# Kernel optimization log

Hardware: AMD Instinct MI355X
Metric: run time of the kernel (lower is better)

The kernel has to match this reference:

```python
import jax, jax.numpy as jnp
import numpy as np

N_NODES = 100000
N_EDGES = 1600000
IN_FEATS = 128
H_FEATS = 128


def setup_inputs() -> dict:
    key = jax.random.key(0)
    ks = jax.random.split(key, 8)
    s_in = 1.0 / np.sqrt(IN_FEATS)
    s_h = 1.0 / np.sqrt(H_FEATS)
    return {
        "emb_weight": jax.random.normal(ks[0], (N_NODES, IN_FEATS), jnp.float32),
        "W1_self": jax.random.normal(ks[1], (IN_FEATS, H_FEATS), jnp.float32) * s_in,
        "W1_neigh": jax.random.normal(ks[2], (IN_FEATS, H_FEATS), jnp.float32) * s_in,
        "b1": jnp.zeros((H_FEATS,), jnp.float32),
        "W2_self": jax.random.normal(ks[3], (H_FEATS, H_FEATS), jnp.float32) * s_h,
        "W2_neigh": jax.random.normal(ks[4], (H_FEATS, H_FEATS), jnp.float32) * s_h,
        "b2": jnp.zeros((H_FEATS,), jnp.float32),
        "edges": jax.random.randint(ks[5], (2, N_EDGES), 0, N_NODES, jnp.int64)
            if jax.config.jax_enable_x64 else
            jax.random.randint(ks[5], (2, N_EDGES), 0, N_NODES, jnp.int32),
    }


def _sage_conv(h, src, dst, W_self, W_neigh, b):
    # DGL SAGEConv(mean): out = h @ W_self + mean_neigh(h) @ W_neigh + b
    agg = jax.ops.segment_sum(h[src], dst, num_segments=N_NODES)  # [N, F]
    deg = jax.ops.segment_sum(jnp.ones((src.shape[0],), h.dtype), dst,
                              num_segments=N_NODES)
    mean = agg / jnp.maximum(deg, 1.0)[:, None]  # zero-in-degree -> zeros
    return h @ W_self + mean @ W_neigh + b


def reference(emb_weight, W1_self, W1_neigh, b1, W2_self, W2_neigh, b2, edges):
    src, dst = edges[0], edges[1]
    h = emb_weight  # node_emb(g.nodes()) over all nodes
    h = _sage_conv(h, src, dst, W1_self, W1_neigh, b1)
    h = jax.nn.leaky_relu(h, negative_slope=0.2)
    # dropout is identity in eval mode
    h = _sage_conv(h, src, dst, W2_self, W2_neigh, b2)
    return h
```

## Files before the change

### kernel.cpp

```cpp
#include <hip/hip_runtime.h>
#include <hip/hip_bf16.h>

#define N_NODES_C 100000
#define FEATS 128
#define SH 10
#define NBK 128
#define PB  256
#define CAST_BLOCKS 12500

typedef unsigned int uint32;
typedef __bf16 bf16_t;
typedef bf16_t bf16x8 __attribute__((ext_vector_type(8)));
typedef float f32x4 __attribute__((ext_vector_type(4)));

union Frag { uint4 u; bf16x8 v; };

__device__ __forceinline__ unsigned short f32_to_bf16_bits(float f) {
    uint32 u = __float_as_uint(f);
    u += 0x7fffu + ((u >> 16) & 1u);
    return (unsigned short)(u >> 16);
}
__device__ __forceinline__ float bf16_lo(uint32 p) { return __uint_as_float(p << 16); }
__device__ __forceinline__ float bf16_hi(uint32 p) { return __uint_as_float(p & 0xffff0000u); }

__global__ __launch_bounds__(256) void prep_fused(
    const int* __restrict__ dst, int* __restrict__ gHist, int nE, int chunk,
    const float4* __restrict__ emb4, unsigned short* __restrict__ hb0, int n4,
    const float* __restrict__ W1s, const float* __restrict__ W1n, unsigned short* __restrict__ wt1,
    const float* __restrict__ W2s, const float* __restrict__ W2n, unsigned short* __restrict__ wt2)
{
    __shared__ int h[NBK];
    const int b = blockIdx.x;
    const int tid = threadIdx.x;

    if (b < PB) {
        if (tid < NBK) h[tid] = 0;
        __syncthreads();
        const int b0 = b * chunk;
        const int e1 = min(b0 + chunk, nE);
        for (int e = b0 + tid; e < e1; e += 256)
            atomicAdd(&h[dst[e] >> SH], 1);
        __syncthreads();
        if (tid < NBK) gHist[tid * PB + b] = h[tid];
    } else if (b < PB + 32) {
        const int which = (b - PB) >> 4;
        const float* Ws = which ? W2s : W1s;
        const float* Wn = which ? W2n : W1n;
        unsigned short* wt = which ? wt2 : wt1;
        int gid = ((b - PB) & 15) * 256 + tid;
        int frag = gid >> 6, lane = gid & 63;
        int nt = frag >> 3, ks = frag & 7;
        int n = nt * 16 + (lane & 15);
        int kbase = ks * 32 + (lane >> 4) * 8;
        union { unsigned short s[8]; uint4 u; } o;
#pragma unroll
        for (int j = 0; j < 8; ++j) {
            int k = kbase + j;
            float v = (k < 128) ? Ws[(size_t)k * FEATS + n] : Wn[(size_t)(k - 128) * FEATS + n];
            o.s[j] = f32_to_bf16_bits(v);
        }
        *(uint4*)(wt + (size_t)gid * 8) = o.u;
    } else {
        int i = (b - PB - 32) * 256 + tid;
        if (i >= n4) return;
        float4 v = emb4[i];
        union { unsigned short s[4]; uint2 u; } o;
        o.s[0] = f32_to_bf16_bits(v.x);
        o.s[1] = f32_to_bf16_bits(v.y);
        o.s[2] = f32_to_bf16_bits(v.z);
        o.s[3] = f32_to_bf16_bits(v.w);
        *(uint2*)(hb0 + (size_t)i * 4) = o.u;
    }
}

__global__ __launch_bounds__(1024) void scan_one(int* __restrict__ g) {
    __shared__ int ss[1024];
    const int tid = threadIdx.x;
    const int base = tid * 32;
    int pref[32];
    int sum = 0;
#pragma unroll
    for (int j = 0; j < 32; ++j) {
        int v = g[base + j];
        pref[j] = sum;
        sum += v;
    }
    ss[tid] = sum;
    __syncthreads();
    for (int d = 1; d < 1024; d <<= 1) {
        int t = (tid >= d) ? ss[tid - d] : 0;
        __syncthreads();
        ss[tid] += t;
        __syncthreads();
    }
    int ex = ss[tid] - sum;
#pragma unroll
    for (int j = 0; j < 32; ++j)
        g[base + j] = ex + pref[j];
}

__global__ __launch_bounds__(256) void part_scatter(const int* __restrict__ src,
                                                    const int* __restrict__ dst,
                                                    const int* __restrict__ gScan,
                                                    uint32* __restrict__ ebuf,
                                                    int nE, int chunk) {
    __shared__ int cur[NBK];
    const int tid = threadIdx.x;
    if (tid < NBK) cur[tid] = gScan[tid * PB + blockIdx.x];
    __syncthreads();
    const int b0 = blockIdx.x * chunk;
    const int e1 = min(b0 + chunk, nE);
    for (int e = b0 + tid; e < e1; e += 256) {
        int d = dst[e];
        int pos = atomicAdd(&cur[d >> SH], 1);
        ebuf[pos] = (uint32)src[e] | ((uint32)(d & ((1 << SH) - 1)) << 17);
    }
}

__global__ __launch_bounds__(1024) void bucket_csr(const uint32* __restrict__ ebuf,
                                                   const int* __restrict__ gScan,
                                                   int* __restrict__ off,
                                                   int* __restrict__ csr,
                                                   int nE) {
    __shared__ int cnt[1 << SH];
    __shared__ int ss[1 << SH];
    const int b = blockIdx.x;
    const int tid = threadIdx.x;
    const int start = gScan[b * PB];
    const int end = gScan[(b + 1) * PB];
    const int nodeBase = b << SH;
    cnt[tid] = 0;
    __syncthreads();
    for (int e = start + tid; e < end; e += 1024)
        atomicAdd(&cnt[ebuf[e] >> 17], 1);
    __syncthreads();
    int own = cnt[tid];
    ss[tid] = own;
    __syncthreads();
    for (int d = 1; d < 1024; d <<= 1) {
        int t = (tid >= d) ? ss[tid - d] : 0;
        __syncthreads();
        ss[tid] += t;
        __syncthreads();
    }
    int ex = ss[tid] - own;
    cnt[tid] = ex;
    int node = nodeBase + tid;
    if (node < N_NODES_C) off[node] = start + ex;
    if (b == gridDim.x - 1 && tid == 0) off[N_NODES_C] = nE;
    __syncthreads();
    for (int e = start + tid; e < end; e += 1024) {
        uint32 p = ebuf[e];
        int pos = atomicAdd(&cnt[p >> 17], 1);
        csr[start + pos] = (int)((p & 0x1FFFFu) << 8);
    }
}

__global__ __launch_bounds__(256) void gather_mean_w2(const unsigned short* __restrict__ hb,
                                                      const int* __restrict__ csrB,
                                                      const int* __restrict__ off,
                                                      unsigned short* __restrict__ meanb,
                                                      int nNodes) {
    const int node = blockIdx.x * 4 + (threadIdx.x >> 6);
    const int lane = threadIdx.x & 63;
    if (node >= nNodes) return;
    const int start = __builtin_amdgcn_readfirstlane(off[node]);
    const int end   = __builtin_amdgcn_readfirstlane(off[node + 1]);
    const int half = lane >> 5;
    const int c = lane & 31;
    const char* base = (const char*)hb + (size_t)(c * 8);
    float a0 = 0.f, a1 = 0.f, a2 = 0.f, a3 = 0.f;
    int e = start;
    for (; e + 8 <= end; e += 8) {
        const int o0 = csrB[e + 0], o1 = csrB[e + 1], o2 = csrB[e + 2], o3 = csrB[e + 3];
        const int o4 = csrB[e + 4], o5 = csrB[e + 5], o6 = csrB[e + 6], o7 = csrB[e + 7];
        const uint2 u0 = *(const uint2*)(base + (size_t)(half ? o1 : o0));
        const uint2 u1 = *(const uint2*)(base + (size_t)(half ? o3 : o2));
        const uint2 u2 = *(const uint2*)(base + (size_t)(half ? o5 : o4));
        const uint2 u3 = *(const uint2*)(base + (size_t)(half ? o7 : o6));
        a0 += bf16_lo(u0.x); a1 += bf16_hi(u0.x); a2 += bf16_lo(u0.y); a3 += bf16_hi(u0.y);
        a0 += bf16_lo(u1.x); a1 += bf16_hi(u1.x); a2 += bf16_lo(u1.y); a3 += bf16_hi(u1.y);
        a0 += bf16_lo(u2.x); a1 += bf16_hi(u2.x); a2 += bf16_lo(u2.y); a3 += bf16_hi(u2.y);
        a0 += bf16_lo(u3.x); a1 += bf16_hi(u3.x); a2 += bf16_lo(u3.y); a3 += bf16_hi(u3.y);
    }
    if (e + 4 <= end) {
        const int o0 = csrB[e + 0], o1 = csrB[e + 1], o2 = csrB[e + 2], o3 = csrB[e + 3];
        const uint2 u0 = *(const uint2*)(base + (size_t)(half ? o1 : o0));
        const uint2 u1 = *(const uint2*)(base + (size_t)(half ? o3 : o2));
        a0 += bf16_lo(u0.x); a1 += bf16_hi(u0.x); a2 += bf16_lo(u0.y); a3 += bf16_hi(u0.y);
        a0 += bf16_lo(u1.x); a1 += bf16_hi(u1.x); a2 += bf16_lo(u1.y); a3 += bf16_hi(u1.y);
        e += 4;
    }
    if (e + 2 <= end) {
        const int o0 = csrB[e + 0], o1 = csrB[e + 1];
        const uint2 u = *(const uint2*)(base + (size_t)(half ? o1 : o0));
        a0 += bf16_lo(u.x); a1 += bf16_hi(u.x); a2 += bf16_lo(u.y); a3 += bf16_hi(u.y);
        e += 2;
    }
    if (e < end && half == 0) {
        const uint2 u = *(const uint2*)(base + (size_t)csrB[e]);
        a0 += bf16_lo(u.x); a1 += bf16_hi(u.x); a2 += bf16_lo(u.y); a3 += bf16_hi(u.y);
    }
    a0 += __shfl_xor(a0, 32);
    a1 += __shfl_xor(a1, 32);
    a2 += __shfl_xor(a2, 32);
    a3 += __shfl_xor(a3, 32);
    const int deg = end - start;
    const float invd = (deg > 0) ? (1.f / (float)deg) : 0.f;
    if (half == 0) {
        uint2 o;
        o.x = ((uint32)f32_to_bf16_bits(a1 * invd) << 16) | (uint32)f32_to_bf16_bits(a0 * invd);
        o.y = ((uint32)f32_to_bf16_bits(a3 * invd) << 16) | (uint32)f32_to_bf16_bits(a2 * invd);
        ((uint2*)meanb)[(size_t)node * 32 + c] = o;
    }
}

__global__ __launch_bounds__(256) void sage_gemm_mfma(const unsigned short* __restrict__ HB,
                                                      const unsigned short* __restrict__ MB,
                                                      const unsigned short* __restrict__ WT,
                                                      const float* __restrict__ bias,
                                                      void* __restrict__ OUTP,
                                                      int nNodes, int mode) {
    const int wave = threadIdx.x >> 6;
    const int lane = threadIdx.x & 63;
    const int waveBase = blockIdx.x * 64 + wave * 16;
    const int m = lane & 15;
    const int quad = lane >> 4;

    int arow = waveBase + m;
    if (arow >= nNodes) arow = nNodes - 1;
    const uint4* hrow = (const uint4*)(HB + (size_t)arow * FEATS);
    const uint4* mrow = (const uint4*)(MB + (size_t)arow * FEATS);

    Frag a[8];
#pragma unroll
    for (int ks = 0; ks < 4; ++ks) a[ks].u = hrow[ks * 4 + quad];
#pragma unroll
    for (int ks = 0; ks < 4; ++ks) a[ks + 4].u = mrow[ks * 4 + quad];

    const uint4* wt4 = (const uint4*)WT;
    f32x4 acc[8];
#pragma unroll
    for (int nt = 0; nt < 8; ++nt) acc[nt] = (f32x4){0.f, 0.f, 0.f, 0.f};

#pragma unroll
    for (int ks = 0; ks < 8; ++ks) {
#pragma unroll
        for (int nt = 0; nt < 8; ++nt) {
            Frag b;
            b.u = wt4[(size_t)(nt * 8 + ks) * 64 + lane];
            acc[nt] = __builtin_amdgcn_mfma_f32_16x16x32_bf16(a[ks].v, b.v, acc[nt], 0, 0, 0);
        }
    }

#pragma unroll
    for (int nt = 0; nt < 8; ++nt) {
        const int col = nt * 16 + m;
        const float bv = bias[col];
#pragma unroll
        for (int r = 0; r < 4; ++r) {
            const int grow = waveBase + quad * 4 + r;
            if (grow >= nNodes) continue;
            float v = acc[nt][r] + bv;
            if (mode) {
                v = v > 0.f ? v : 0.2f * v;
                ((unsigned short*)OUTP)[(size_t)grow * FEATS + col] = f32_to_bf16_bits(v);
            } else {
                ((float*)OUTP)[(size_t)grow * FEATS + col] = v;
            }
        }
    }
}

extern "C" void kernel_launch(void* const* d_in, const int* in_sizes, int n_in,
                              void* d_out, int out_size, void* d_ws, size_t ws_size,
                              hipStream_t stream) {
    const float* emb = (const float*)d_in[0];
    const float* W1s = (const float*)d_in[1];
    const float* W1n = (const float*)d_in[2];
    const float* b1  = (const float*)d_in[3];
    const float* W2s = (const float*)d_in[4];
    const float* W2n = (const float*)d_in[5];
    const float* b2  = (const float*)d_in[6];
    const int*   edg = (const int*)d_in[7];

    const int nE = in_sizes[7] / 2;
    const int* src = edg;
    const int* dst = edg + nE;

    const int chunk = (nE + PB - 1) / PB;
    const int nActB = (N_NODES_C + (1 << SH) - 1) >> SH;
    const int n4 = N_NODES_C * FEATS / 4;

    const size_t bfTab = (size_t)N_NODES_C * FEATS * sizeof(unsigned short);

    char* ws = (char*)d_ws;
    int* off      = (int*)(ws);
    int* gHist    = (int*)(ws + (512 << 10));
    int* csr      = (int*)(ws + (1 << 20));
    uint32* ebuf  = (uint32*)(ws + (8 << 20));
    unsigned short* wt1 = (unsigned short*)(ws + (15 << 20));
    unsigned short* wt2 = (unsigned short*)(ws + (15 << 20) + (64 << 10));
    unsigned short* hb0 = (unsigned short*)(ws + (16 << 20));
    unsigned short* h1b = (unsigned short*)((char*)hb0 + bfTab);
    unsigned short* mnb = (unsigned short*)((char*)h1b + bfTab);
    float* out = (float*)d_out;

    prep_fused<<<PB + 32 + CAST_BLOCKS, 256, 0, stream>>>(
        dst, gHist, nE, chunk, (const float4*)emb, hb0, n4,
        W1s, W1n, wt1, W2s, W2n, wt2);

    scan_one<<<1, 1024, 0, stream>>>(gHist);
    part_scatter<<<PB, 256, 0, stream>>>(src, dst, gHist, ebuf, nE, chunk);
    bucket_csr<<<nActB, 1024, 0, stream>>>(ebuf, gHist, off, csr, nE);

    const int gatherBlocks = (N_NODES_C + 3) / 4;
    const int gemmBlocks = (N_NODES_C + 63) / 64;

    gather_mean_w2<<<gatherBlocks, 256, 0, stream>>>(hb0, csr, off, mnb, N_NODES_C);
    sage_gemm_mfma<<<gemmBlocks, 256, 0, stream>>>(hb0, mnb, wt1, b1, h1b, N_NODES_C, 1);

    gather_mean_w2<<<gatherBlocks, 256, 0, stream>>>(h1b, csr, off, mnb, N_NODES_C);
    sage_gemm_mfma<<<gemmBlocks, 256, 0, stream>>>(h1b, mnb, wt2, b2, out, N_NODES_C, 0);
}
```

Before: 349.3 us.

## Widen scatter blocks, unroll gather by 16, and compute two row tiles per GEMM wave

Three independent changes. The partition scatter now runs 1024 threads per block instead of 256, giving more parallelism per chunk. The neighbor gather loop is unrolled to 16 edges per iteration so more independent loads are in flight. The MFMA GEMM now has each wave handle 32 rows (two 16-row tiles) that share each weight fragment load, halving the weight traffic per row at the cost of more registers and half as many blocks.

```diff
diff --git a/kernel.cpp b/kernel.cpp
--- a/kernel.cpp
+++ b/kernel.cpp
@@ -99,18 +99,18 @@
         g[base + j] = ex + pref[j];
 }
 
-__global__ __launch_bounds__(256) void part_scatter(const int* __restrict__ src,
-                                                    const int* __restrict__ dst,
-                                                    const int* __restrict__ gScan,
-                                                    uint32* __restrict__ ebuf,
-                                                    int nE, int chunk) {
+__global__ __launch_bounds__(1024) void part_scatter(const int* __restrict__ src,
+                                                     const int* __restrict__ dst,
+                                                     const int* __restrict__ gScan,
+                                                     uint32* __restrict__ ebuf,
+                                                     int nE, int chunk) {
     __shared__ int cur[NBK];
     const int tid = threadIdx.x;
     if (tid < NBK) cur[tid] = gScan[tid * PB + blockIdx.x];
     __syncthreads();
     const int b0 = blockIdx.x * chunk;
     const int e1 = min(b0 + chunk, nE);
-    for (int e = b0 + tid; e < e1; e += 256) {
+    for (int e = b0 + tid; e < e1; e += 1024) {
         int d = dst[e];
         int pos = atomicAdd(&cur[d >> SH], 1);
         ebuf[pos] = (uint32)src[e] | ((uint32)(d & ((1 << SH) - 1)) << 17);
@@ -171,7 +171,29 @@
     const char* base = (const char*)hb + (size_t)(c * 8);
     float a0 = 0.f, a1 = 0.f, a2 = 0.f, a3 = 0.f;
     int e = start;
-    for (; e + 8 <= end; e += 8) {
+    for (; e + 16 <= end; e += 16) {
+        const int o0  = csrB[e + 0],  o1  = csrB[e + 1],  o2  = csrB[e + 2],  o3  = csrB[e + 3];
+        const int o4  = csrB[e + 4],  o5  = csrB[e + 5],  o6  = csrB[e + 6],  o7  = csrB[e + 7];
+        const int o8  = csrB[e + 8],  o9  = csrB[e + 9],  o10 = csrB[e + 10], o11 = csrB[e + 11];
+        const int o12 = csrB[e + 12], o13 = csrB[e + 13], o14 = csrB[e + 14], o15 = csrB[e + 15];
+        const uint2 u0 = *(const uint2*)(base + (size_t)(half ? o1  : o0));
+        const uint2 u1 = *(const uint2*)(base + (size_t)(half ? o3  : o2));
+        const uint2 u2 = *(const uint2*)(base + (size_t)(half ? o5  : o4));
+        const uint2 u3 = *(const uint2*)(base + (size_t)(half ? o7  : o6));
+        const uint2 u4 = *(const uint2*)(base + (size_t)(half ? o9  : o8));
+        const uint2 u5 = *(const uint2*)(base + (size_t)(half ? o11 : o10));
+        const uint2 u6 = *(const uint2*)(base + (size_t)(half ? o13 : o12));
+        const uint2 u7 = *(const uint2*)(base + (size_t)(half ? o15 : o14));
+        a0 += bf16_lo(u0.x); a1 += bf16_hi(u0.x); a2 += bf16_lo(u0.y); a3 += bf16_hi(u0.y);
+        a0 += bf16_lo(u1.x); a1 += bf16_hi(u1.x); a2 += bf16_lo(u1.y); a3 += bf16_hi(u1.y);
+        a0 += bf16_lo(u2.x); a1 += bf16_hi(u2.x); a2 += bf16_lo(u2.y); a3 += bf16_hi(u2.y);
+        a0 += bf16_lo(u3.x); a1 += bf16_hi(u3.x); a2 += bf16_lo(u3.y); a3 += bf16_hi(u3.y);
+        a0 += bf16_lo(u4.x); a1 += bf16_hi(u4.x); a2 += bf16_lo(u4.y); a3 += bf16_hi(u4.y);
+        a0 += bf16_lo(u5.x); a1 += bf16_hi(u5.x); a2 += bf16_lo(u5.y); a3 += bf16_hi(u5.y);
+        a0 += bf16_lo(u6.x); a1 += bf16_hi(u6.x); a2 += bf16_lo(u6.y); a3 += bf16_hi(u6.y);
+        a0 += bf16_lo(u7.x); a1 += bf16_hi(u7.x); a2 += bf16_lo(u7.y); a3 += bf16_hi(u7.y);
+    }
+    if (e + 8 <= end) {
         const int o0 = csrB[e + 0], o1 = csrB[e + 1], o2 = csrB[e + 2], o3 = csrB[e + 3];
         const int o4 = csrB[e + 4], o5 = csrB[e + 5], o6 = csrB[e + 6], o7 = csrB[e + 7];
         const uint2 u0 = *(const uint2*)(base + (size_t)(half ? o1 : o0));
@@ -182,6 +204,7 @@
         a0 += bf16_lo(u1.x); a1 += bf16_hi(u1.x); a2 += bf16_lo(u1.y); a3 += bf16_hi(u1.y);
         a0 += bf16_lo(u2.x); a1 += bf16_hi(u2.x); a2 += bf16_lo(u2.y); a3 += bf16_hi(u2.y);
         a0 += bf16_lo(u3.x); a1 += bf16_hi(u3.x); a2 += bf16_lo(u3.y); a3 += bf16_hi(u3.y);
+        e += 8;
     }
     if (e + 4 <= end) {
         const int o0 = csrB[e + 0], o1 = csrB[e + 1], o2 = csrB[e + 2], o3 = csrB[e + 3];
@@ -223,25 +246,36 @@
                                                       int nNodes, int mode) {
     const int wave = threadIdx.x >> 6;
     const int lane = threadIdx.x & 63;
-    const int waveBase = blockIdx.x * 64 + wave * 16;
+    const int waveBase = blockIdx.x * 128 + wave * 32;
     const int m = lane & 15;
     const int quad = lane >> 4;
 
-    int arow = waveBase + m;
-    if (arow >= nNodes) arow = nNodes - 1;
-    const uint4* hrow = (const uint4*)(HB + (size_t)arow * FEATS);
-    const uint4* mrow = (const uint4*)(MB + (size_t)arow * FEATS);
-
-    Frag a[8];
-#pragma unroll
-    for (int ks = 0; ks < 4; ++ks) a[ks].u = hrow[ks * 4 + quad];
-#pragma unroll
-    for (int ks = 0; ks < 4; ++ks) a[ks + 4].u = mrow[ks * 4 + quad];
+    int arow0 = waveBase + m;
+    int arow1 = waveBase + 16 + m;
+    if (arow0 >= nNodes) arow0 = nNodes - 1;
+    if (arow1 >= nNodes) arow1 = nNodes - 1;
+    const uint4* hrow0 = (const uint4*)(HB + (size_t)arow0 * FEATS);
+    const uint4* mrow0 = (const uint4*)(MB + (size_t)arow0 * FEATS);
+    const uint4* hrow1 = (const uint4*)(HB + (size_t)arow1 * FEATS);
+    const uint4* mrow1 = (const uint4*)(MB + (size_t)arow1 * FEATS);
+
+    Frag a0[8], a1[8];
+#pragma unroll
+    for (int ks = 0; ks < 4; ++ks) a0[ks].u = hrow0[ks * 4 + quad];
+#pragma unroll
+    for (int ks = 0; ks < 4; ++ks) a0[ks + 4].u = mrow0[ks * 4 + quad];
+#pragma unroll
+    for (int ks = 0; ks < 4; ++ks) a1[ks].u = hrow1[ks * 4 + quad];
+#pragma unroll
+    for (int ks = 0; ks < 4; ++ks) a1[ks + 4].u = mrow1[ks * 4 + quad];
 
     const uint4* wt4 = (const uint4*)WT;
-    f32x4 acc[8];
-#pragma unroll
-    for (int nt = 0; nt < 8; ++nt) acc[nt] = (f32x4){0.f, 0.f, 0.f, 0.f};
+    f32x4 acc0[8], acc1[8];
+#pragma unroll
+    for (int nt = 0; nt < 8; ++nt) {
+        acc0[nt] = (f32x4){0.f, 0.f, 0.f, 0.f};
+        acc1[nt] = (f32x4){0.f, 0.f, 0.f, 0.f};
+    }
 
 #pragma unroll
     for (int ks = 0; ks < 8; ++ks) {
@@ -249,7 +283,8 @@
         for (int nt = 0; nt < 8; ++nt) {
             Frag b;
             b.u = wt4[(size_t)(nt * 8 + ks) * 64 + lane];
-            acc[nt] = __builtin_amdgcn_mfma_f32_16x16x32_bf16(a[ks].v, b.v, acc[nt], 0, 0, 0);
+            acc0[nt] = __builtin_amdgcn_mfma_f32_16x16x32_bf16(a0[ks].v, b.v, acc0[nt], 0, 0, 0);
+            acc1[nt] = __builtin_amdgcn_mfma_f32_16x16x32_bf16(a1[ks].v, b.v, acc1[nt], 0, 0, 0);
         }
     }
 
@@ -259,14 +294,25 @@
         const float bv = bias[col];
 #pragma unroll
         for (int r = 0; r < 4; ++r) {
-            const int grow = waveBase + quad * 4 + r;
-            if (grow >= nNodes) continue;
-            float v = acc[nt][r] + bv;
-            if (mode) {
-                v = v > 0.f ? v : 0.2f * v;
-                ((unsigned short*)OUTP)[(size_t)grow * FEATS + col] = f32_to_bf16_bits(v);
-            } else {
-                ((float*)OUTP)[(size_t)grow * FEATS + col] = v;
+            const int g0 = waveBase + quad * 4 + r;
+            const int g1 = waveBase + 16 + quad * 4 + r;
+            if (g0 < nNodes) {
+                float v = acc0[nt][r] + bv;
+                if (mode) {
+                    v = v > 0.f ? v : 0.2f * v;
+                    ((unsigned short*)OUTP)[(size_t)g0 * FEATS + col] = f32_to_bf16_bits(v);
+                } else {
+                    ((float*)OUTP)[(size_t)g0 * FEATS + col] = v;
+                }
+            }
+            if (g1 < nNodes) {
+                float v = acc1[nt][r] + bv;
+                if (mode) {
+                    v = v > 0.f ? v : 0.2f * v;
+                    ((unsigned short*)OUTP)[(size_t)g1 * FEATS + col] = f32_to_bf16_bits(v);
+                } else {
+                    ((float*)OUTP)[(size_t)g1 * FEATS + col] = v;
+                }
             }
         }
     }
@@ -311,11 +357,11 @@
         W1s, W1n, wt1, W2s, W2n, wt2);
 
     scan_one<<<1, 1024, 0, stream>>>(gHist);
-    part_scatter<<<PB, 256, 0, stream>>>(src, dst, gHist, ebuf, nE, chunk);
+    part_scatter<<<PB, 1024, 0, stream>>>(src, dst, gHist, ebuf, nE, chunk);
     bucket_csr<<<nActB, 1024, 0, stream>>>(ebuf, gHist, off, csr, nE);
 
     const int gatherBlocks = (N_NODES_C + 3) / 4;
-    const int gemmBlocks = (N_NODES_C + 63) / 64;
+    const int gemmBlocks = (N_NODES_C + 127) / 128;
 
     gather_mean_w2<<<gatherBlocks, 256, 0, stream>>>(hb0, csr, off, mnb, N_NODES_C);
     sage_gemm_mfma<<<gemmBlocks, 256, 0, stream>>>(hb0, mnb, wt1, b1, h1b, N_NODES_C, 1);
```

New measurement: 385.3 us. +10.3%, slower.
